# Performance work log

Hardware: AMD Instinct MI355X
Metric: run time of the kernel (lower is better)

The kernel has to match this reference:

```python
import jax, jax.numpy as jnp
import numpy as np

D_MODEL = 512
N_HEADS = 8
D_K = D_MODEL // N_HEADS
LN_EPS = 1e-5


def setup_inputs() -> dict:
    key = jax.random.key(0)
    ks = jax.random.split(key, 8)
    B, S, D = 2, 4096, D_MODEL
    # xavier_uniform bound for square [D, D] weight
    bound = float(np.sqrt(6.0 / (D + D)))
    x = jax.random.normal(ks[0], (B, S, D), dtype=jnp.float32)
    w_q = jax.random.uniform(ks[1], (D, D), jnp.float32, -bound, bound)
    w_k = jax.random.uniform(ks[2], (D, D), jnp.float32, -bound, bound)
    w_v = jax.random.uniform(ks[3], (D, D), jnp.float32, -bound, bound)
    # w_o: torch Linear default init (kaiming-uniform-ish); uniform is fine as data
    lim = float(1.0 / np.sqrt(D))
    w_o = jax.random.uniform(ks[4], (D, D), jnp.float32, -lim, lim)
    b_o = jax.random.uniform(ks[5], (D,), jnp.float32, -lim, lim)
    ln_gamma = jnp.ones((D,), jnp.float32)
    ln_beta = jnp.zeros((D,), jnp.float32)
    return {"x": x, "w_q": w_q, "w_k": w_k, "w_v": w_v,
            "w_o": w_o, "b_o": b_o, "ln_gamma": ln_gamma, "ln_beta": ln_beta}


def _layer_norm(x, gamma, beta):
    mu = jnp.mean(x, axis=-1, keepdims=True)
    var = jnp.mean(jnp.square(x - mu), axis=-1, keepdims=True)
    return (x - mu) * jax.lax.rsqrt(var + LN_EPS) * gamma + beta


def reference(x, w_q, w_k, w_v, w_o, b_o, ln_gamma, ln_beta):
    B, S, D = x.shape
    residual = x
    h = _layer_norm(x, ln_gamma, ln_beta)
    # torch Linear: y = h @ W.T ; reshape to [B, H, S, d_k]
    def proj(W):
        return (h @ W.T).reshape(B, S, N_HEADS, D_K).transpose(0, 2, 1, 3)
    Q, K, V = proj(w_q), proj(w_k), proj(w_v)
    scores = jnp.einsum('bhqd,bhkd->bhqk', Q, K) / jnp.sqrt(jnp.float32(D_K))
    attn = jax.nn.softmax(scores, axis=-1)  # dropout p=0 -> identity
    attended = jnp.einsum('bhqk,bhkd->bhqd', attn, V)
    attended = attended.transpose(0, 2, 1, 3).reshape(B, S, D)
    out = attended @ w_o.T + b_o
    return out + residual
```

## Files before the change

kernel.cpp:

```cpp
#include <hip/hip_runtime.h>
#include <hip/hip_bf16.h>
#include <stdint.h>


typedef __bf16 bf16;
typedef __attribute__((ext_vector_type(8))) __bf16 bf16x8;
typedef __attribute__((ext_vector_type(4))) __bf16 bf16x4;
typedef __attribute__((ext_vector_type(4))) float f32x4;
typedef __attribute__((ext_vector_type(4))) unsigned int u32x4;

#define LOG2E 1.44269504088896340736f
#define SW(row, grp) (((row) << 6) + ((((grp) ^ ((row) & 7))) << 3))

__device__ __forceinline__ unsigned int pkbf16(float lo, float hi) {
  return __builtin_amdgcn_perm(__builtin_bit_cast(unsigned int, hi),
                               __builtin_bit_cast(unsigned int, lo),
                               0x07060302u);
}

__global__ __launch_bounds__(256) void ln_kernel(
    const float* __restrict__ x, const float* __restrict__ gamma,
    const float* __restrict__ beta, bf16* __restrict__ h) {
  int wave = threadIdx.x >> 6, lane = threadIdx.x & 63;
  int row = blockIdx.x * 4 + wave;
  const float* xr = x + (size_t)row * 512 + lane * 8;
  f32x4 v0 = *(const f32x4*)xr;
  f32x4 v1 = *(const f32x4*)(xr + 4);
  float f[8], s = 0.f, s2 = 0.f;
#pragma unroll
  for (int i = 0; i < 4; ++i) { f[i] = v0[i]; f[4 + i] = v1[i]; }
#pragma unroll
  for (int i = 0; i < 8; ++i) { s += f[i]; s2 += f[i] * f[i]; }
#pragma unroll
  for (int off = 1; off < 64; off <<= 1) {
    s  += __shfl_xor(s, off, 64);
    s2 += __shfl_xor(s2, off, 64);
  }
  float mu  = s * (1.f / 512.f);
  float var = s2 * (1.f / 512.f) - mu * mu;
  float rstd = rsqrtf(var + 1e-5f);
  f32x4 g0 = *(const f32x4*)(gamma + lane * 8);
  f32x4 g1 = *(const f32x4*)(gamma + lane * 8 + 4);
  f32x4 b0 = *(const f32x4*)(beta + lane * 8);
  f32x4 b1 = *(const f32x4*)(beta + lane * 8 + 4);
  bf16x8 o;
#pragma unroll
  for (int i = 0; i < 4; ++i) {
    o[i]     = (bf16)((f[i]     - mu) * rstd * g0[i] + b0[i]);
    o[4 + i] = (bf16)((f[4 + i] - mu) * rstd * g1[i] + b1[i]);
  }
  *(bf16x8*)(h + (size_t)row * 512 + lane * 8) = o;
}

__global__ __launch_bounds__(256) void qkv_kernel(
    const bf16* __restrict__ h, const float* __restrict__ wq,
    const float* __restrict__ wk, const float* __restrict__ wv,
    bf16* __restrict__ Qg, bf16* __restrict__ Kg, bf16* __restrict__ Vtg) {
  __shared__ bf16 As[128 * 64];
  __shared__ bf16 Bs[128 * 64];
  int tid = threadIdx.x, wave = tid >> 6, lane = tid & 63;
  int wm = wave >> 1, wn = wave & 1, quad = lane >> 4, l15 = lane & 15;
  int lin = blockIdx.x + (blockIdx.y << 6);
  int xcd = lin & 7, idx = lin >> 3;
  int mtile = xcd * 8 + idx / 12;
  int yy = idx % 12;
  int wsel = yy >> 2;
  int nb = yy & 3;
  const float* W = (wsel == 0) ? wq : (wsel == 1 ? wk : wv);
  const bf16*  Abase = h + (size_t)mtile * 128 * 512;
  const float* Bbase = W + (size_t)nb * 128 * 512;
  f32x4 acc[4][4];
#pragma unroll
  for (int i = 0; i < 4; ++i)
#pragma unroll
    for (int j = 0; j < 4; ++j) acc[i][j] = (f32x4){0.f, 0.f, 0.f, 0.f};

  int srow = tid >> 3, grp = tid & 7, scol = grp * 8;
  bf16x8 ar[4];
  f32x4 br0[4], br1[4];
#pragma unroll
  for (int k = 0; k < 4; ++k) {
    int rr = srow + k * 32;
    ar[k]  = *(const bf16x8*)(Abase + (size_t)rr * 512 + scol);
    br0[k] = *(const f32x4*)(Bbase + (size_t)rr * 512 + scol);
    br1[k] = *(const f32x4*)(Bbase + (size_t)rr * 512 + scol + 4);
  }
  for (int k0 = 0; k0 < 512; k0 += 64) {
#pragma unroll
    for (int k = 0; k < 4; ++k) {
      int rr = srow + k * 32;
      int w = SW(rr, grp);
      *(bf16x8*)(As + w) = ar[k];
      bf16x8 wb;
#pragma unroll
      for (int j = 0; j < 4; ++j) { wb[j] = (bf16)br0[k][j]; wb[4 + j] = (bf16)br1[k][j]; }
      *(bf16x8*)(Bs + w) = wb;
    }
    __syncthreads();
    if (k0 < 448) {
#pragma unroll
      for (int k = 0; k < 4; ++k) {
        int rr = srow + k * 32;
        ar[k]  = *(const bf16x8*)(Abase + (size_t)rr * 512 + k0 + 64 + scol);
        br0[k] = *(const f32x4*)(Bbase + (size_t)rr * 512 + k0 + 64 + scol);
        br1[k] = *(const f32x4*)(Bbase + (size_t)rr * 512 + k0 + 64 + scol + 4);
      }
    }
#pragma unroll
    for (int c = 0; c < 2; ++c) {
      bf16x8 af[4], bw[4];
#pragma unroll
      for (int mt = 0; mt < 4; ++mt)
        af[mt] = *(const bf16x8*)(As + SW(wm * 64 + mt * 16 + l15, c * 4 + quad));
#pragma unroll
      for (int nt = 0; nt < 4; ++nt)
        bw[nt] = *(const bf16x8*)(Bs + SW(wn * 64 + nt * 16 + l15, c * 4 + quad));
#pragma unroll
      for (int mt = 0; mt < 4; ++mt)
#pragma unroll
        for (int nt = 0; nt < 4; ++nt)
          acc[mt][nt] = __builtin_amdgcn_mfma_f32_16x16x32_bf16(
              bw[nt], af[mt], acc[mt][nt], 0, 0, 0);
    }
    __syncthreads();
  }
  float qscale = (wsel == 0) ? (0.125f * LOG2E) : 1.0f;
#pragma unroll
  for (int mt = 0; mt < 4; ++mt) {
    int m_g = mtile * 128 + wm * 64 + mt * 16 + l15;
    int b = m_g >> 12, s = m_g & 4095;
#pragma unroll
    for (int nt = 0; nt < 4; ++nt) {
      int n_g = nb * 128 + wn * 64 + nt * 16 + quad * 4;
      int head = n_g >> 6, d = n_g & 63;
      f32x4 a = acc[mt][nt];
      if (wsel < 2) {
        bf16* dst = (wsel == 0 ? Qg : Kg) +
                    ((size_t)((b * 8 + head) * 4096 + s)) * 64 + d;
        bf16x4 pk;
#pragma unroll
        for (int r = 0; r < 4; ++r) pk[r] = (bf16)(a[r] * qscale);
        *(bf16x4*)dst = pk;
      } else {
        bf16* dst = Vtg + ((size_t)((b * 8 + head) * 64 + d)) * 4096 + s;
#pragma unroll
        for (int r = 0; r < 4; ++r) dst[(size_t)r * 4096] = (bf16)a[r];
      }
    }
  }
}

__device__ __forceinline__ void write_kv_tile(bf16* dst, const bf16x8* sr,
                                              int qgrp, int lane) {
  if (!qgrp) {
#pragma unroll
    for (int i = 0; i < 8; ++i) {
      int e = i * 512 + lane * 8;
      *(bf16x8*)(dst + SW(e >> 6, (e >> 3) & 7)) = sr[i];
    }
  } else {
#pragma unroll
    for (int i = 0; i < 8; ++i) {
      int e = i * 512 + lane * 8;
      int row = e >> 6, g = (e >> 3) & 7;
      int pr = g >> 2, s = (g >> 1) & 1, gq = g & 1;
      bf16x4 lo, hi;
#pragma unroll
      for (int j = 0; j < 4; ++j) { lo[j] = sr[i][j]; hi[j] = sr[i][4 + j]; }
      *(bf16x4*)(dst + SW(row, pr * 4 + gq * 2)     + s * 4) = lo;
      *(bf16x4*)(dst + SW(row, pr * 4 + gq * 2 + 1) + s * 4) = hi;
    }
  }
}

__global__ __launch_bounds__(256, 2) void attn_kernel(
    const bf16* __restrict__ Qg, const bf16* __restrict__ Kg,
    const bf16* __restrict__ Vtg, bf16* __restrict__ Og) {
  __shared__ char smem[64 * 1024];
  bf16* KV = (bf16*)smem;
  float* OL = (float*)smem;
  float* Ll = (float*)(smem + 49152);

  int tid = threadIdx.x, wave = tid >> 6, lane = tid & 63;
  int quad = lane >> 4, l15 = lane & 15;
  int qgrp = wave & 1, khalf = wave >> 1;
  int lin = blockIdx.x;
  int bh = ((lin & 7) << 1) | ((lin >> 3) & 1);
  int q0 = (lin >> 4) * 128;
  int hi = bh & 7, bi = bh >> 3;
  const bf16* Kh  = Kg  + (size_t)bh * 4096 * 64;
  const bf16* Vth = Vtg + (size_t)bh * 64 * 4096;

  bf16x8 qf[4][2];
#pragma unroll
  for (int mt = 0; mt < 4; ++mt)
#pragma unroll
    for (int c = 0; c < 2; ++c)
      qf[mt][c] = *(const bf16x8*)(
          Qg + ((size_t)bh * 4096 + q0 + qgrp * 64 + mt * 16 + l15) * 64 +
          c * 32 + quad * 8);

  f32x4 o_acc[4][4], lacc[4];
#pragma unroll
  for (int mt = 0; mt < 4; ++mt) {
    lacc[mt] = (f32x4){0.f, 0.f, 0.f, 0.f};
#pragma unroll
    for (int nt = 0; nt < 4; ++nt) o_acc[mt][nt] = (f32x4){0.f, 0.f, 0.f, 0.f};
  }
  const u32x4 onesu = {0x3F803F80u, 0x3F803F80u, 0x3F803F80u, 0x3F803F80u};
  const bf16x8 ones8 = __builtin_bit_cast(bf16x8, onesu);
  const f32x4 z4 = {0.f, 0.f, 0.f, 0.f};

  bf16* sbase = KV + khalf * 8192 + (qgrp ? 4096 : 0);
  bf16x8 sr[8];
  int key0 = khalf * 2048;
#pragma unroll
  for (int i = 0; i < 8; ++i) {
    int e = i * 512 + lane * 8;
    sr[i] = qgrp
        ? *(const bf16x8*)(Vth + (size_t)(e >> 6) * 4096 + key0 + (e & 63))
        : *(const bf16x8*)(Kh + (size_t)key0 * 64 + e);
  }
  write_kv_tile(sbase, sr, qgrp, lane);
#pragma unroll
  for (int i = 0; i < 8; ++i) {
    int e = i * 512 + lane * 8;
    sr[i] = qgrp
        ? *(const bf16x8*)(Vth + (size_t)(e >> 6) * 4096 + key0 + 64 + (e & 63))
        : *(const bf16x8*)(Kh + (size_t)(key0 + 64) * 64 + e);
  }
  __syncthreads();

  for (int kt = 0; kt < 32; ++kt) {
    int cur = kt & 1, nxt = cur ^ 1;
    bf16* Ksw = KV + cur * 16384 + khalf * 8192;
    bf16* Vsw = Ksw + 4096;
    if (kt < 31) {
      write_kv_tile(sbase + nxt * 16384, sr, qgrp, lane);
    }
    if (kt < 30) {
      int kbase = key0 + (kt + 2) * 64;
#pragma unroll
      for (int i = 0; i < 8; ++i) {
        int e = i * 512 + lane * 8;
        sr[i] = qgrp
            ? *(const bf16x8*)(Vth + (size_t)(e >> 6) * 4096 + kbase + (e & 63))
            : *(const bf16x8*)(Kh + (size_t)kbase * 64 + e);
      }
    }
    bf16x8 kf[8];
#pragma unroll
    for (int kb = 0; kb < 4; ++kb)
#pragma unroll
      for (int c = 0; c < 2; ++c)
        kf[kb * 2 + c] = *(const bf16x8*)(Ksw + SW(kb * 16 + l15, c * 4 + quad));
    bf16x8 vf8[2][4];
#pragma unroll
    for (int pr = 0; pr < 2; ++pr)
#pragma unroll
      for (int nt = 0; nt < 4; ++nt)
        vf8[pr][nt] = *(const bf16x8*)(Vsw + SW(nt * 16 + l15, pr * 4 + quad));
#pragma unroll
    for (int mt = 0; mt < 4; ++mt) {
      f32x4 st[4];
      __builtin_amdgcn_s_setprio(1);
#pragma unroll
      for (int kb = 0; kb < 4; ++kb)
        st[kb] = __builtin_amdgcn_mfma_f32_16x16x32_bf16(
            kf[kb * 2], qf[mt][0], z4, 0, 0, 0);
#pragma unroll
      for (int kb = 0; kb < 4; ++kb)
        st[kb] = __builtin_amdgcn_mfma_f32_16x16x32_bf16(
            kf[kb * 2 + 1], qf[mt][1], st[kb], 0, 0, 0);
      __builtin_amdgcn_s_setprio(0);
#pragma unroll
      for (int pr = 0; pr < 2; ++pr) {
        float ea[4], eb[4];
#pragma unroll
        for (int r = 0; r < 4; ++r) {
          ea[r] = __builtin_amdgcn_exp2f(st[pr * 2][r]);
          eb[r] = __builtin_amdgcn_exp2f(st[pr * 2 + 1][r]);
        }
        u32x4 pw = {pkbf16(ea[0], ea[1]), pkbf16(ea[2], ea[3]),
                    pkbf16(eb[0], eb[1]), pkbf16(eb[2], eb[3])};
        bf16x8 pk8 = __builtin_bit_cast(bf16x8, pw);
        __builtin_amdgcn_s_setprio(1);
#pragma unroll
        for (int nt = 0; nt < 4; ++nt)
          o_acc[mt][nt] = __builtin_amdgcn_mfma_f32_16x16x32_bf16(
              vf8[pr][nt], pk8, o_acc[mt][nt], 0, 0, 0);
        lacc[mt] = __builtin_amdgcn_mfma_f32_16x16x32_bf16(
            ones8, pk8, lacc[mt], 0, 0, 0);
        __builtin_amdgcn_s_setprio(0);
      }
    }
    __syncthreads();
  }
  if (khalf == 1) {
    float* dst = OL + qgrp * 4096;
#pragma unroll
    for (int mt = 0; mt < 4; ++mt) {
#pragma unroll
      for (int nt = 0; nt < 4; ++nt) {
        int row = mt * 16 + l15;
        int g = nt * 4 + quad;
        int gs = (g & 8) | ((g ^ row) & 7);
        *(f32x4*)(&dst[row * 64 + gs * 4]) = o_acc[mt][nt];
      }
      if (quad == 0) Ll[qgrp * 64 + mt * 16 + l15] = lacc[mt][0];
    }
  }
  __syncthreads();
  if (khalf == 0) {
    const float* src = OL + qgrp * 4096;
#pragma unroll
    for (int mt = 0; mt < 4; ++mt) {
      float lt = lacc[mt][0] + Ll[qgrp * 64 + mt * 16 + l15];
      float inv = 1.0f / lt;
      int q = q0 + qgrp * 64 + mt * 16 + l15;
#pragma unroll
      for (int nt = 0; nt < 4; ++nt) {
        int row = mt * 16 + l15;
        int g = nt * 4 + quad;
        int gs = (g & 8) | ((g ^ row) & 7);
        f32x4 o = *(const f32x4*)(&src[row * 64 + gs * 4]);
        bf16x4 pk;
#pragma unroll
        for (int r = 0; r < 4; ++r)
          pk[r] = (bf16)((o[r] + o_acc[mt][nt][r]) * inv);
        *(bf16x4*)(&Og[((size_t)bi * 4096 + q) * 512 + hi * 64 + nt * 16 +
                       quad * 4]) = pk;
      }
    }
  }
}

__global__ __launch_bounds__(256) void proj_kernel(
    const bf16* __restrict__ A, const float* __restrict__ Wo,
    const float* __restrict__ bo, const float* __restrict__ x,
    float* __restrict__ out) {
  __shared__ bf16 As[128 * 64];
  __shared__ bf16 Bs[128 * 64];
  int tid = threadIdx.x, wave = tid >> 6, lane = tid & 63;
  int wm = wave >> 1, wn = wave & 1, quad = lane >> 4, l15 = lane & 15;
  int mtile = blockIdx.x, nb = blockIdx.y;
  const bf16*  Abase = A + (size_t)mtile * 128 * 512;
  const float* Bbase = Wo + (size_t)nb * 128 * 512;
  f32x4 acc[4][4];
#pragma unroll
  for (int i = 0; i < 4; ++i)
#pragma unroll
    for (int j = 0; j < 4; ++j) acc[i][j] = (f32x4){0.f, 0.f, 0.f, 0.f};

  int srow = tid >> 3, grp = tid & 7, scol = grp * 8;
  bf16x8 ar[4];
  f32x4 br0[4], br1[4];
#pragma unroll
  for (int k = 0; k < 4; ++k) {
    int rr = srow + k * 32;
    ar[k]  = *(const bf16x8*)(Abase + (size_t)rr * 512 + scol);
    br0[k] = *(const f32x4*)(Bbase + (size_t)rr * 512 + scol);
    br1[k] = *(const f32x4*)(Bbase + (size_t)rr * 512 + scol + 4);
  }
  for (int k0 = 0; k0 < 512; k0 += 64) {
#pragma unroll
    for (int k = 0; k < 4; ++k) {
      int rr = srow + k * 32;
      int w = SW(rr, grp);
      *(bf16x8*)(As + w) = ar[k];
      bf16x8 wb;
#pragma unroll
      for (int j = 0; j < 4; ++j) { wb[j] = (bf16)br0[k][j]; wb[4 + j] = (bf16)br1[k][j]; }
      *(bf16x8*)(Bs + w) = wb;
    }
    __syncthreads();
    if (k0 < 448) {
#pragma unroll
      for (int k = 0; k < 4; ++k) {
        int rr = srow + k * 32;
        ar[k]  = *(const bf16x8*)(Abase + (size_t)rr * 512 + k0 + 64 + scol);
        br0[k] = *(const f32x4*)(Bbase + (size_t)rr * 512 + k0 + 64 + scol);
        br1[k] = *(const f32x4*)(Bbase + (size_t)rr * 512 + k0 + 64 + scol + 4);
      }
    }
#pragma unroll
    for (int c = 0; c < 2; ++c) {
      bf16x8 af[4], bw[4];
#pragma unroll
      for (int mt = 0; mt < 4; ++mt)
        af[mt] = *(const bf16x8*)(As + SW(wm * 64 + mt * 16 + l15, c * 4 + quad));
#pragma unroll
      for (int nt = 0; nt < 4; ++nt)
        bw[nt] = *(const bf16x8*)(Bs + SW(wn * 64 + nt * 16 + l15, c * 4 + quad));
#pragma unroll
      for (int mt = 0; mt < 4; ++mt)
#pragma unroll
        for (int nt = 0; nt < 4; ++nt)
          acc[mt][nt] = __builtin_amdgcn_mfma_f32_16x16x32_bf16(
              bw[nt], af[mt], acc[mt][nt], 0, 0, 0);
    }
    __syncthreads();
  }
#pragma unroll
  for (int mt = 0; mt < 4; ++mt) {
    int m_g = mtile * 128 + wm * 64 + mt * 16 + l15;
#pragma unroll
    for (int nt = 0; nt < 4; ++nt) {
      int n_g = nb * 128 + wn * 64 + nt * 16 + quad * 4;
      f32x4 a = acc[mt][nt];
      f32x4 xr = *(const f32x4*)(x + (size_t)m_g * 512 + n_g);
      f32x4 bb = *(const f32x4*)(bo + n_g);
      f32x4 o;
#pragma unroll
      for (int r = 0; r < 4; ++r)
        o[r] = a[r] + bb[r] + xr[r];
      *(f32x4*)(out + (size_t)m_g * 512 + n_g) = o;
    }
  }
}

extern "C" void kernel_launch(void* const* d_in, const int* in_sizes, int n_in,
                              void* d_out, int out_size, void* d_ws, size_t ws_size,
                              hipStream_t stream) {
  const float* x     = (const float*)d_in[0];
  const float* wq    = (const float*)d_in[1];
  const float* wk    = (const float*)d_in[2];
  const float* wv    = (const float*)d_in[3];
  const float* wo    = (const float*)d_in[4];
  const float* bo    = (const float*)d_in[5];
  const float* gamma = (const float*)d_in[6];
  const float* beta  = (const float*)d_in[7];
  float* out = (float*)d_out;
  char* ws = (char*)d_ws;
  const size_t SZ = (size_t)8192 * 512 * sizeof(bf16);
  bf16* h   = (bf16*)(ws);
  bf16* Ao  = (bf16*)(ws);
  bf16* Qg  = (bf16*)(ws + SZ);
  bf16* Kg  = (bf16*)(ws + 2 * SZ);
  bf16* Vtg = (bf16*)(ws + 3 * SZ);

  ln_kernel<<<2048, 256, 0, stream>>>(x, gamma, beta, h);
  qkv_kernel<<<dim3(64, 12), 256, 0, stream>>>(h, wq, wk, wv, Qg, Kg, Vtg);
  attn_kernel<<<512, 256, 0, stream>>>(Qg, Kg, Vtg, Ao);
  proj_kernel<<<dim3(64, 4), 256, 0, stream>>>(Ao, wo, bo, x, out);
}
```

Measured before the change: 190.4 us.

## Load K/V tiles via global_load_lds and pre-permute V layout in QKV epilogue

The attention kernel now streams K and V tiles straight from global memory into LDS with global_load_lds, replacing the register staging and the swizzled LDS writes. The swizzle is applied on the global address side. To make a direct copy line up with the V fragment layout, the QKV kernel's V epilogue transposes the tile through shared memory and writes Vt with the interleaved column order the attention MFMA reads expect. The s_setprio hints are also dropped. This saves VGPRs and VALU work in the attention loop, at the cost of extra LDS traffic and a sync in the QKV epilogue.

```diff
diff --git a/kernel.cpp b/kernel.cpp
--- a/kernel.cpp
+++ b/kernel.cpp
@@ -16,6 +16,12 @@
   return __builtin_amdgcn_perm(__builtin_bit_cast(unsigned int, hi),
                                __builtin_bit_cast(unsigned int, lo),
                                0x07060302u);
+}
+
+__device__ __forceinline__ void gl_lds16(const bf16* g, bf16* l) {
+  __builtin_amdgcn_global_load_lds(
+      (const __attribute__((address_space(1))) void*)g,
+      (__attribute__((address_space(3))) void*)l, 16, 0, 0);
 }
 
 __global__ __launch_bounds__(256) void ln_kernel(
@@ -56,8 +62,9 @@
     const bf16* __restrict__ h, const float* __restrict__ wq,
     const float* __restrict__ wk, const float* __restrict__ wv,
     bf16* __restrict__ Qg, bf16* __restrict__ Kg, bf16* __restrict__ Vtg) {
-  __shared__ bf16 As[128 * 64];
-  __shared__ bf16 Bs[128 * 64];
+  __shared__ bf16 smemq[2 * 128 * 64];
+  bf16* As = smemq;
+  bf16* Bs = smemq + 128 * 64;
   int tid = threadIdx.x, wave = tid >> 6, lane = tid & 63;
   int wm = wave >> 1, wn = wave & 1, quad = lane >> 4, l15 = lane & 15;
   int lin = blockIdx.x + (blockIdx.y << 6);
@@ -124,51 +131,57 @@
     }
     __syncthreads();
   }
-  float qscale = (wsel == 0) ? (0.125f * LOG2E) : 1.0f;
-#pragma unroll
-  for (int mt = 0; mt < 4; ++mt) {
-    int m_g = mtile * 128 + wm * 64 + mt * 16 + l15;
-    int b = m_g >> 12, s = m_g & 4095;
-#pragma unroll
-    for (int nt = 0; nt < 4; ++nt) {
-      int n_g = nb * 128 + wn * 64 + nt * 16 + quad * 4;
-      int head = n_g >> 6, d = n_g & 63;
-      f32x4 a = acc[mt][nt];
-      if (wsel < 2) {
+  if (wsel < 2) {
+    float qscale = (wsel == 0) ? (0.125f * LOG2E) : 1.0f;
+#pragma unroll
+    for (int mt = 0; mt < 4; ++mt) {
+      int m_g = mtile * 128 + wm * 64 + mt * 16 + l15;
+      int b = m_g >> 12, s = m_g & 4095;
+#pragma unroll
+      for (int nt = 0; nt < 4; ++nt) {
+        int n_g = nb * 128 + wn * 64 + nt * 16 + quad * 4;
+        int head = n_g >> 6, d = n_g & 63;
+        f32x4 a = acc[mt][nt];
         bf16* dst = (wsel == 0 ? Qg : Kg) +
                     ((size_t)((b * 8 + head) * 4096 + s)) * 64 + d;
         bf16x4 pk;
 #pragma unroll
         for (int r = 0; r < 4; ++r) pk[r] = (bf16)(a[r] * qscale);
         *(bf16x4*)dst = pk;
-      } else {
-        bf16* dst = Vtg + ((size_t)((b * 8 + head) * 64 + d)) * 4096 + s;
-#pragma unroll
-        for (int r = 0; r < 4; ++r) dst[(size_t)r * 4096] = (bf16)a[r];
-      }
-    }
-  }
-}
-
-__device__ __forceinline__ void write_kv_tile(bf16* dst, const bf16x8* sr,
-                                              int qgrp, int lane) {
-  if (!qgrp) {
-#pragma unroll
-    for (int i = 0; i < 8; ++i) {
-      int e = i * 512 + lane * 8;
-      *(bf16x8*)(dst + SW(e >> 6, (e >> 3) & 7)) = sr[i];
+      }
     }
   } else {
-#pragma unroll
-    for (int i = 0; i < 8; ++i) {
-      int e = i * 512 + lane * 8;
-      int row = e >> 6, g = (e >> 3) & 7;
-      int pr = g >> 2, s = (g >> 1) & 1, gq = g & 1;
-      bf16x4 lo, hi;
-#pragma unroll
-      for (int j = 0; j < 4; ++j) { lo[j] = sr[i][j]; hi[j] = sr[i][4 + j]; }
-      *(bf16x4*)(dst + SW(row, pr * 4 + gq * 2)     + s * 4) = lo;
-      *(bf16x4*)(dst + SW(row, pr * 4 + gq * 2 + 1) + s * 4) = hi;
+    bf16* Vt = smemq;
+#pragma unroll
+    for (int mt = 0; mt < 4; ++mt) {
+      int t = wm * 64 + mt * 16 + l15;
+#pragma unroll
+      for (int nt = 0; nt < 4; ++nt) {
+#pragma unroll
+        for (int r = 0; r < 4; ++r) {
+          int f = wn * 64 + nt * 16 + quad * 4 + r;
+          Vt[f * 128 + (t ^ ((f & 7) << 3))] = (bf16)acc[mt][nt][r];
+        }
+      }
+    }
+    __syncthreads();
+    int fr = tid >> 1, hf = tid & 1;
+    int n_g = nb * 128 + fr;
+    int head = n_g >> 6, d = n_g & 63;
+    int bb = mtile >> 5;
+    bf16* dst = Vtg + ((size_t)((bb * 8 + head) * 64 + d)) * 4096 +
+                (mtile & 31) * 128 + hf * 64;
+    int sx3 = (fr & 7) << 3;
+#pragma unroll
+    for (int g = 0; g < 8; ++g) {
+      int pr = g >> 2, qd = g & 3;
+      int tb = hf * 64 + pr * 32 + qd * 4;
+      bf16x4 lo  = *(const bf16x4*)(Vt + fr * 128 + (tb ^ sx3));
+      bf16x4 hi4 = *(const bf16x4*)(Vt + fr * 128 + ((tb + 16) ^ sx3));
+      bf16x8 v;
+#pragma unroll
+      for (int j = 0; j < 4; ++j) { v[j] = lo[j]; v[4 + j] = hi4[j]; }
+      *(bf16x8*)(dst + g * 8) = v;
     }
   }
 }
@@ -211,23 +224,20 @@
   const bf16x8 ones8 = __builtin_bit_cast(bf16x8, onesu);
   const f32x4 z4 = {0.f, 0.f, 0.f, 0.f};
 
-  bf16* sbase = KV + khalf * 8192 + (qgrp ? 4096 : 0);
-  bf16x8 sr[8];
   int key0 = khalf * 2048;
-#pragma unroll
-  for (int i = 0; i < 8; ++i) {
-    int e = i * 512 + lane * 8;
-    sr[i] = qgrp
-        ? *(const bf16x8*)(Vth + (size_t)(e >> 6) * 4096 + key0 + (e & 63))
-        : *(const bf16x8*)(Kh + (size_t)key0 * 64 + e);
-  }
-  write_kv_tile(sbase, sr, qgrp, lane);
-#pragma unroll
-  for (int i = 0; i < 8; ++i) {
-    int e = i * 512 + lane * 8;
-    sr[i] = qgrp
-        ? *(const bf16x8*)(Vth + (size_t)(e >> 6) * 4096 + key0 + 64 + (e & 63))
-        : *(const bf16x8*)(Kh + (size_t)(key0 + 64) * 64 + e);
+  int lr = lane >> 3, lg = (lane & 7) ^ (lr & 7);
+  const bf16* gKb = Kh + ((size_t)key0 + lr) * 64 + lg * 8;
+  const bf16* gVb = Vth + (size_t)lr * 4096 + key0 + lg * 8;
+  bf16* myK = KV + khalf * 8192;
+  bf16* myV = myK + 4096;
+
+  if (qgrp == 0) {
+#pragma unroll
+    for (int i = 0; i < 8; ++i) gl_lds16(gKb + i * 512, myK + i * 512);
+  } else {
+#pragma unroll
+    for (int i = 0; i < 8; ++i)
+      gl_lds16(gVb + (size_t)i * 32768, myV + i * 512);
   }
   __syncthreads();
 
@@ -236,16 +246,17 @@
     bf16* Ksw = KV + cur * 16384 + khalf * 8192;
     bf16* Vsw = Ksw + 4096;
     if (kt < 31) {
-      write_kv_tile(sbase + nxt * 16384, sr, qgrp, lane);
-    }
-    if (kt < 30) {
-      int kbase = key0 + (kt + 2) * 64;
-#pragma unroll
-      for (int i = 0; i < 8; ++i) {
-        int e = i * 512 + lane * 8;
-        sr[i] = qgrp
-            ? *(const bf16x8*)(Vth + (size_t)(e >> 6) * 4096 + kbase + (e & 63))
-            : *(const bf16x8*)(Kh + (size_t)kbase * 64 + e);
+      if (qgrp == 0) {
+        const bf16* src = gKb + (size_t)(kt + 1) * 4096;
+        bf16* d = myK + nxt * 16384;
+#pragma unroll
+        for (int i = 0; i < 8; ++i) gl_lds16(src + i * 512, d + i * 512);
+      } else {
+        const bf16* src = gVb + (kt + 1) * 64;
+        bf16* d = myV + nxt * 16384;
+#pragma unroll
+        for (int i = 0; i < 8; ++i)
+          gl_lds16(src + (size_t)i * 32768, d + i * 512);
       }
     }
     bf16x8 kf[8];
@@ -263,7 +274,6 @@
 #pragma unroll
     for (int mt = 0; mt < 4; ++mt) {
       f32x4 st[4];
-      __builtin_amdgcn_s_setprio(1);
 #pragma unroll
       for (int kb = 0; kb < 4; ++kb)
         st[kb] = __builtin_amdgcn_mfma_f32_16x16x32_bf16(
@@ -272,7 +282,6 @@
       for (int kb = 0; kb < 4; ++kb)
         st[kb] = __builtin_amdgcn_mfma_f32_16x16x32_bf16(
             kf[kb * 2 + 1], qf[mt][1], st[kb], 0, 0, 0);
-      __builtin_amdgcn_s_setprio(0);
 #pragma unroll
       for (int pr = 0; pr < 2; ++pr) {
         float ea[4], eb[4];
@@ -284,14 +293,12 @@
         u32x4 pw = {pkbf16(ea[0], ea[1]), pkbf16(ea[2], ea[3]),
                     pkbf16(eb[0], eb[1]), pkbf16(eb[2], eb[3])};
         bf16x8 pk8 = __builtin_bit_cast(bf16x8, pw);
-        __builtin_amdgcn_s_setprio(1);
 #pragma unroll
         for (int nt = 0; nt < 4; ++nt)
           o_acc[mt][nt] = __builtin_amdgcn_mfma_f32_16x16x32_bf16(
               vf8[pr][nt], pk8, o_acc[mt][nt], 0, 0, 0);
         lacc[mt] = __builtin_amdgcn_mfma_f32_16x16x32_bf16(
             ones8, pk8, lacc[mt], 0, 0, 0);
-        __builtin_amdgcn_s_setprio(0);
       }
     }
     __syncthreads();
```

Result: faster. 185.6 us (-2.5%).
